# Optimization experiments

Measured on AMD Instinct MI355X. Metric: run time of the kernel, lower is better.

Reference implementation:

```python
import jax, jax.numpy as jnp
import numpy as np

B, T, C = 4, 2048, 2048
H = 16
D = C // H  # 128


def setup_inputs() -> dict:
    key = jax.random.key(0)
    ks = jax.random.split(key, 9)
    s = 0.02
    return {
        "x": jax.random.normal(ks[0], (B, T, C), dtype=jnp.float32),
        "wq": jax.random.normal(ks[1], (C, C), dtype=jnp.float32) * s,
        "bq": jax.random.normal(ks[2], (C,), dtype=jnp.float32) * s,
        "wk": jax.random.normal(ks[3], (C, C), dtype=jnp.float32) * s,
        "bk": jax.random.normal(ks[4], (C,), dtype=jnp.float32) * s,
        "wv": jax.random.normal(ks[5], (C, C), dtype=jnp.float32) * s,
        "bv": jax.random.normal(ks[6], (C,), dtype=jnp.float32) * s,
        "wo": jax.random.normal(ks[7], (C, C), dtype=jnp.float32) * s,
        "bo": jax.random.normal(ks[8], (C,), dtype=jnp.float32) * s,
    }


def reference(x, wq, bq, wk, bk, wv, bv, wo, bo):
    Bz, Tz, Cz = x.shape
    # projections (torch Linear: x @ W^T + b)
    q = (x @ wq.T + bq).reshape(Bz, Tz, H, D).transpose(0, 2, 1, 3)  # [B,H,T,D]
    k = (x @ wk.T + bk).reshape(Bz, Tz, H, D).transpose(0, 2, 1, 3)
    v = (x @ wv.T + bv).reshape(Bz, Tz, H, D).transpose(0, 2, 1, 3)
    scale = 1.0 / jnp.sqrt(jnp.float32(D))
    scores = jnp.einsum("bhqd,bhkd->bhqk", q, k) * scale  # [B,H,T,T]
    causal = jnp.tril(jnp.ones((Tz, Tz), dtype=bool))
    scores = jnp.where(causal, scores, jnp.float32(-jnp.inf))
    att = jax.nn.softmax(scores, axis=-1)
    out = jnp.einsum("bhqk,bhkd->bhqd", att, v)  # [B,H,T,D]
    out = out.transpose(0, 2, 1, 3).reshape(Bz, Tz, Cz)
    out = out @ wo.T + bo
    return out
```

## Files before the change

### kernel.cpp

```cpp
#include <hip/hip_runtime.h>
#include <hip/hip_bf16.h>

typedef float  f32x4  __attribute__((ext_vector_type(4)));
typedef __bf16 bf16x8 __attribute__((ext_vector_type(8)));
typedef __bf16 bf16x4 __attribute__((ext_vector_type(4)));

#define Bz 4
#define Tz 2048
#define Cz 2048
#define Hh 16
#define Dd 128
#define Mm 8192

__device__ __forceinline__ void gload_lds16(const __bf16* g, __bf16* l) {
  __builtin_amdgcn_global_load_lds(
      (const __attribute__((address_space(1))) void*)g,
      (__attribute__((address_space(3))) void*)l, 16, 0, 0);
}

__global__ __launch_bounds__(256)
void cvt_bf16(const float* __restrict__ in, __bf16* __restrict__ out, int n8) {
  int i = blockIdx.x * 256 + threadIdx.x;
  if (i >= n8) return;
  size_t base = (size_t)i * 8;
  f32x4 a = *(const f32x4*)(in + base);
  f32x4 b = *(const f32x4*)(in + base + 4);
  bf16x8 o;
  o[0]=(__bf16)a[0]; o[1]=(__bf16)a[1]; o[2]=(__bf16)a[2]; o[3]=(__bf16)a[3];
  o[4]=(__bf16)b[0]; o[5]=(__bf16)b[1]; o[6]=(__bf16)b[2]; o[7]=(__bf16)b[3];
  *(bf16x8*)(out + base) = o;
}

template<int MODE>
__global__ __launch_bounds__(512, 2)
void gemm_bt(const __bf16* __restrict__ A, const __bf16* __restrict__ W,
             const float* __restrict__ bias, void* __restrict__ Out,
             int K, float scale)
{
  __shared__ __bf16 As[2][256 * 64];
  __shared__ __bf16 Bs[2][256 * 64];

  const int tid  = threadIdx.x;
  const int lane = tid & 63;
  const int wave = tid >> 6;
  const int wm = wave >> 2, wn = wave & 3;
  const int g  = lane >> 4;
  const int lr = lane & 15;
  const int row0 = blockIdx.x * 256;
  const int col0 = blockIdx.y * 256;

  #define STG(MAT, PTR, base0, kofs, buf)                                \
    _Pragma("unroll")                                                    \
    for (int q = 0; q < 4; ++q) {                                        \
      const int r  = q * 64 + (tid >> 3);                                \
      const int cb = (tid & 7) ^ (r & 7);                                \
      gload_lds16(PTR + (size_t)(base0 + r) * K + (kofs) + cb * 8,       \
                  &MAT[buf][(q * 64 + wave * 8) * 64]);                  \
    }

  f32x4 acc[8][4] = {};

  STG(As, A, row0, 0, 0);
  STG(Bs, W, col0, 0, 0);
  asm volatile("s_waitcnt vmcnt(0)" ::: "memory");
  asm volatile("s_barrier" ::: "memory");

  const int NT = K >> 6;
  bf16x8 bfr[4][2];
  for (int kt = 0; kt < NT; ++kt) {
    const int d  = kt & 1;
    const bool pf = (kt + 1 < NT);
    const int kn = (kt + 1) << 6;

    #pragma unroll
    for (int p = 0; p < 4; ++p) {
      if (p == 0) {
        #pragma unroll
        for (int n = 0; n < 4; ++n)
          #pragma unroll
          for (int kk = 0; kk < 2; ++kk) {
            const int br = wn * 64 + n * 16 + lr;
            bfr[n][kk] = *(const bf16x8*)(&Bs[d][br * 64 + ((((kk << 2) | g) ^ (br & 7)) << 3)]);
          }
      }
      bf16x8 af[2][2];
      #pragma unroll
      for (int mf = 0; mf < 2; ++mf)
        #pragma unroll
        for (int kk = 0; kk < 2; ++kk) {
          const int ar = wm * 128 + (p * 2 + mf) * 16 + lr;
          af[mf][kk] = *(const bf16x8*)(&As[d][ar * 64 + ((((kk << 2) | g) ^ (ar & 7)) << 3)]);
        }
      if (pf && p == 0) STG(As, A, row0, kn, d ^ 1);
      if (pf && p == 1) STG(Bs, W, col0, kn, d ^ 1);

      asm volatile("s_barrier" ::: "memory");
      __builtin_amdgcn_s_setprio(1);
      #pragma unroll
      for (int kk = 0; kk < 2; ++kk)
        #pragma unroll
        for (int mf = 0; mf < 2; ++mf)
          #pragma unroll
          for (int n = 0; n < 4; ++n)
            acc[p * 2 + mf][n] = __builtin_amdgcn_mfma_f32_16x16x32_bf16(
                af[mf][kk], bfr[n][kk], acc[p * 2 + mf][n], 0, 0, 0);
      __builtin_amdgcn_s_setprio(0);
      if (p == 3) asm volatile("s_waitcnt vmcnt(0)" ::: "memory");
      asm volatile("s_barrier" ::: "memory");
    }
  }
  #undef STG

  #pragma unroll
  for (int j = 0; j < 4; ++j) {
    const int col = col0 + wn * 64 + j * 16 + lr;
    const float bv = bias[col];
    #pragma unroll
    for (int i = 0; i < 8; ++i) {
      if (MODE == 2) {
        const int row = row0 + wm * 128 + i * 16 + g * 4;
        const int b = row >> 11, t = row & (Tz - 1);
        const int h = col >> 7,  d = col & (Dd - 1);
        bf16x4 v4;
        #pragma unroll
        for (int r = 0; r < 4; ++r) v4[r] = (__bf16)(acc[i][j][r] + bv);
        *(bf16x4*)((__bf16*)Out + ((size_t)(b * Hh + h) * Dd + d) * Tz + t) = v4;
      } else {
        #pragma unroll
        for (int r = 0; r < 4; ++r) {
          const int row = row0 + wm * 128 + i * 16 + g * 4 + r;
          const float v = acc[i][j][r] + bv;
          if (MODE == 0) {
            const int b = row >> 11, t = row & (Tz - 1);
            const int h = col >> 7,  d = col & (Dd - 1);
            ((__bf16*)Out)[((size_t)(b * Hh + h) * Tz + t) * Dd + d] = (__bf16)(v * scale);
          } else {
            ((float*)Out)[(size_t)row * Cz + col] = v;
          }
        }
      }
    }
  }
}

__global__ __launch_bounds__(256, 2)
void attn_fwd(const __bf16* __restrict__ Q, const __bf16* __restrict__ Kg,
              const __bf16* __restrict__ Vt, __bf16* __restrict__ O)
{
  __shared__ __bf16 Ks[2][64 * 128];
  __shared__ __bf16 Vs[2][128 * 64];
  __shared__ __bf16 Ps[4][32 * 64];

  const int tid  = threadIdx.x;
  const int lane = tid & 63;
  const int wave = tid >> 6;
  const int g  = lane >> 4;
  const int lr = lane & 15;
  const int pair = blockIdx.y;
  const int b = pair >> 4, h = pair & 15;

  const __bf16* Qp = Q  + (size_t)pair * Tz * Dd;
  const __bf16* Kp = Kg + (size_t)pair * Tz * Dd;
  const __bf16* Vp = Vt + (size_t)pair * Dd * Tz;

  #define STAGE_KV(kv0_, buf_)                                                  \
    {                                                                           \
      const int kv0s = (kv0_);                                                  \
      _Pragma("unroll")                                                         \
      for (int p = 0; p < 4; ++p) {                                             \
        const int r  = p * 16 + wave * 4 + (lane >> 4);                         \
        const int cb = (lane & 15) ^ (r & 7);                                   \
        gload_lds16(Kp + (size_t)(kv0s + r) * Dd + cb * 8,                      \
                    &Ks[buf_][p * 2048 + wave * 512]);                          \
        const int d  = p * 32 + wave * 8 + (lane >> 3);                         \
        const int cv = (lane & 7) ^ (d & 7);                                    \
        gload_lds16(Vp + (size_t)d * Tz + kv0s + cv * 8,                        \
                    &Vs[buf_][p * 2048 + wave * 512]);                          \
      }                                                                         \
    }

  for (int pass = 0; pass < 2; ++pass) {
    const int qt  = pass == 0 ? (15 - (int)blockIdx.x) : (int)blockIdx.x;
    const int qw0 = qt * 128 + wave * 32;

    bf16x8 qf[2][4];
    #pragma unroll
    for (int im = 0; im < 2; ++im)
      #pragma unroll
      for (int ks = 0; ks < 4; ++ks)
        qf[im][ks] = *(const bf16x8*)(Qp + (size_t)(qw0 + im*16 + lr) * Dd + ks*32 + g*8);

    f32x4 oacc[2][8] = {};
    float mrow[2], lsum[2];
    mrow[0] = mrow[1] = -1e30f;
    lsum[0] = lsum[1] = 0.f;

    const int ntiles = 2 * qt + 2;

    STAGE_KV(0, 0);
    __syncthreads();

    for (int kt = 0; kt < ntiles; ++kt) {
      const int cur = kt & 1;
      const int kv0 = kt * 64;
      if (kt + 1 < ntiles) STAGE_KV((kt + 1) * 64, cur ^ 1);

      if (kv0 <= qw0 + 31) {
        f32x4 sacc[2][4] = {};
        __builtin_amdgcn_s_setprio(1);
        #pragma unroll
        for (int ks = 0; ks < 4; ++ks) {
          bf16x8 kf[4];
          #pragma unroll
          for (int in = 0; in < 4; ++in) {
            const int r = in*16 + lr;
            kf[in] = *(const bf16x8*)(&Ks[cur][r * 128 + ((((ks<<2)|g) ^ (r & 7)) << 3)]);
          }
          #pragma unroll
          for (int im = 0; im < 2; ++im)
            #pragma unroll
            for (int in = 0; in < 4; ++in)
              sacc[im][in] = __builtin_amdgcn_mfma_f32_16x16x32_bf16(kf[in], qf[im][ks], sacc[im][in], 0, 0, 0);
        }
        __builtin_amdgcn_s_setprio(0);

        if (kv0 + 63 > qw0) {
          #pragma unroll
          for (int im = 0; im < 2; ++im) {
            const int q = qw0 + im*16 + lr;
            #pragma unroll
            for (int in = 0; in < 4; ++in)
              #pragma unroll
              for (int r = 0; r < 4; ++r) {
                const int kv = kv0 + in*16 + g*4 + r;
                if (kv > q) sacc[im][in][r] = -3e38f;
              }
          }
        }

        #pragma unroll
        for (int im = 0; im < 2; ++im) {
          float m = fmaxf(fmaxf(sacc[im][0][0], sacc[im][0][1]),
                          fmaxf(sacc[im][0][2], sacc[im][0][3]));
          #pragma unroll
          for (int in = 1; in < 4; ++in)
            m = fmaxf(m, fmaxf(fmaxf(sacc[im][in][0], sacc[im][in][1]),
                               fmaxf(sacc[im][in][2], sacc[im][in][3])));
          m = fmaxf(m, __shfl_xor(m, 16));
          m = fmaxf(m, __shfl_xor(m, 32));

          const bool need = m > mrow[im] + 11.54f;
          if (__any(need)) {
            const float mn   = need ? m : mrow[im];
            const float corr = __builtin_amdgcn_exp2f(mrow[im] - mn);
            mrow[im] = mn;
            lsum[im] *= corr;
            const int sb = 20 * g;
            const float c0 = __shfl(corr, sb + 0);
            const float c1 = __shfl(corr, sb + 1);
            const float c2 = __shfl(corr, sb + 2);
            const float c3 = __shfl(corr, sb + 3);
            #pragma unroll
            for (int dn = 0; dn < 8; ++dn) {
              oacc[im][dn][0] *= c0; oacc[im][dn][1] *= c1;
              oacc[im][dn][2] *= c2; oacc[im][dn][3] *= c3;
            }
          }

          float rs = 0.f;
          const int prow = im*16 + lr;
          #pragma unroll
          for (int in = 0; in < 4; ++in) {
            const float p0 = __builtin_amdgcn_exp2f(sacc[im][in][0] - mrow[im]);
            const float p1 = __builtin_amdgcn_exp2f(sacc[im][in][1] - mrow[im]);
            const float p2 = __builtin_amdgcn_exp2f(sacc[im][in][2] - mrow[im]);
            const float p3 = __builtin_amdgcn_exp2f(sacc[im][in][3] - mrow[im]);
            rs += (p0 + p1) + (p2 + p3);
            bf16x4 q4;
            q4[0] = (__bf16)p0; q4[1] = (__bf16)p1;
            q4[2] = (__bf16)p2; q4[3] = (__bf16)p3;
            const int bs = (in*4 + g) ^ ((prow & 3) << 2);
            *(bf16x4*)(&Ps[wave][prow * 64 + bs * 4]) = q4;
          }
          rs += __shfl_xor(rs, 16);
          rs += __shfl_xor(rs, 32);
          lsum[im] += rs;
        }

        __builtin_amdgcn_s_setprio(1);
        #pragma unroll
        for (int kk = 0; kk < 2; ++kk) {
          bf16x8 pa[2];
          #pragma unroll
          for (int im = 0; im < 2; ++im) {
            const int prow = im*16 + lr;
            const int bs = (kk*8 + 2*g) ^ ((prow & 3) << 2);
            pa[im] = *(const bf16x8*)(&Ps[wave][prow * 64 + bs * 4]);
          }
          #pragma unroll
          for (int dn = 0; dn < 8; ++dn) {
            const int d = dn*16 + lr;
            bf16x8 vb = *(const bf16x8*)(&Vs[cur][d * 64 + ((((kk<<2)|g) ^ (d & 7)) << 3)]);
            #pragma unroll
            for (int im = 0; im < 2; ++im)
              oacc[im][dn] = __builtin_amdgcn_mfma_f32_16x16x32_bf16(pa[im], vb, oacc[im][dn], 0, 0, 0);
          }
        }
        __builtin_amdgcn_s_setprio(0);
      }
      __syncthreads();
    }

    #pragma unroll
    for (int im = 0; im < 2; ++im) {
      const float inv = 1.0f / lsum[im];
      const int sb = 20 * g;
      const float i0 = __shfl(inv, sb + 0);
      const float i1 = __shfl(inv, sb + 1);
      const float i2 = __shfl(inv, sb + 2);
      const float i3 = __shfl(inv, sb + 3);
      #pragma unroll
      for (int dn = 0; dn < 8; ++dn) {
        const int qrow = qw0 + im*16 + g*4;
        const int d    = h * Dd + dn*16 + lr;
        O[((size_t)(b * Tz + qrow + 0)) * Cz + d] = (__bf16)(oacc[im][dn][0] * i0);
        O[((size_t)(b * Tz + qrow + 1)) * Cz + d] = (__bf16)(oacc[im][dn][1] * i1);
        O[((size_t)(b * Tz + qrow + 2)) * Cz + d] = (__bf16)(oacc[im][dn][2] * i2);
        O[((size_t)(b * Tz + qrow + 3)) * Cz + d] = (__bf16)(oacc[im][dn][3] * i3);
      }
    }
  }
  #undef STAGE_KV
}

extern "C" void kernel_launch(void* const* d_in, const int* in_sizes, int n_in,
                              void* d_out, int out_size, void* d_ws, size_t ws_size,
                              hipStream_t stream) {
  const float* x  = (const float*)d_in[0];
  const float* wq = (const float*)d_in[1];
  const float* bq = (const float*)d_in[2];
  const float* wk = (const float*)d_in[3];
  const float* bk = (const float*)d_in[4];
  const float* wv = (const float*)d_in[5];
  const float* bv = (const float*)d_in[6];
  const float* wo = (const float*)d_in[7];
  const float* bo = (const float*)d_in[8];
  float* out = (float*)d_out;

  char* w = (char*)d_ws;
  __bf16* xb   = (__bf16*)w; w += (size_t)Mm * Cz * 2;
  __bf16* wbuf = (__bf16*)w; w += (size_t)Cz * Cz * 2;
  __bf16* qb   = (__bf16*)w; w += (size_t)Mm * Cz * 2;
  __bf16* kb   = (__bf16*)w; w += (size_t)Mm * Cz * 2;
  __bf16* vbuf = (__bf16*)w; w += (size_t)Mm * Cz * 2;
  if (ws_size < (size_t)(w - (char*)d_ws)) return;

  const int nx8 = Mm * Cz / 8;
  const int nw8 = Cz * Cz / 8;
  dim3 ggrid(Mm / 256, Cz / 256);
  const float qscale = 0.12752551286084110f;

  cvt_bf16<<<nx8 / 256, 256, 0, stream>>>(x, xb, nx8);

  cvt_bf16<<<nw8 / 256, 256, 0, stream>>>(wq, wbuf, nw8);
  gemm_bt<0><<<ggrid, 512, 0, stream>>>(xb, wbuf, bq, qb, Cz, qscale);

  cvt_bf16<<<nw8 / 256, 256, 0, stream>>>(wk, wbuf, nw8);
  gemm_bt<0><<<ggrid, 512, 0, stream>>>(xb, wbuf, bk, kb, Cz, 1.0f);

  cvt_bf16<<<nw8 / 256, 256, 0, stream>>>(wv, wbuf, nw8);
  gemm_bt<2><<<ggrid, 512, 0, stream>>>(xb, wbuf, bv, vbuf, Cz, 1.0f);

  __bf16* ob = xb;
  attn_fwd<<<dim3(8, Bz * Hh), 256, 0, stream>>>(qb, kb, vbuf, ob);

  cvt_bf16<<<nw8 / 256, 256, 0, stream>>>(wo, wbuf, nw8);
  gemm_bt<1><<<ggrid, 512, 0, stream>>>(ob, wbuf, bo, out, Cz, 1.0f);
}
```

Before: 423.0 us.

## Restructure GEMM LDS staging into per-half buffers with two-stage-ahead prefetch

The GEMM's LDS tiles are split into 128-row halves, so each wave group loads only the half it consumes. Global-to-LDS loads are now issued two k-tiles ahead, with a partial vmcnt wait, instead of one tile ahead inside the compute phases. The goal is to hide more global memory latency and keep loads off the MFMA phases. The cost is an extra barrier and vmcnt wait after each k-tile, plus more loads in flight.

```diff
diff --git a/kernel.cpp b/kernel.cpp
--- a/kernel.cpp
+++ b/kernel.cpp
@@ -37,8 +37,8 @@
              const float* __restrict__ bias, void* __restrict__ Out,
              int K, float scale)
 {
-  __shared__ __bf16 As[2][256 * 64];
-  __shared__ __bf16 Bs[2][256 * 64];
+  __shared__ __bf16 Ah[4][128 * 64];
+  __shared__ __bf16 Bh[4][128 * 64];
 
   const int tid  = threadIdx.x;
   const int lane = tid & 63;
@@ -49,29 +49,37 @@
   const int row0 = blockIdx.x * 256;
   const int col0 = blockIdx.y * 256;
 
-  #define STG(MAT, PTR, base0, kofs, buf)                                \
-    _Pragma("unroll")                                                    \
-    for (int q = 0; q < 4; ++q) {                                        \
-      const int r  = q * 64 + (tid >> 3);                                \
-      const int cb = (tid & 7) ^ (r & 7);                                \
-      gload_lds16(PTR + (size_t)(base0 + r) * K + (kofs) + cb * 8,       \
-                  &MAT[buf][(q * 64 + wave * 8) * 64]);                  \
+  const int hb  = wn >> 1;
+  const int sbB = wm * 2 + (wn & 1);
+  const int cbl = ((lane & 7) ^ (lane >> 3)) << 3;
+  const int rlA = lane >> 3;
+
+  #define STAGE(s_)                                                          \
+    {                                                                        \
+      const int buf_ = (((s_) & 1) << 1);                                    \
+      const int ko_  = (s_) << 6;                                            \
+      _Pragma("unroll")                                                      \
+      for (int j = 0; j < 4; ++j) {                                          \
+        const int rA_ = wn * 32 + j * 8;                                     \
+        gload_lds16(A + (size_t)(row0 + wm * 128 + rA_ + rlA) * K + ko_ + cbl,\
+                    &Ah[buf_ + wm][rA_ * 64]);                               \
+        const int rB_ = sbB * 32 + j * 8;                                    \
+        gload_lds16(W + (size_t)(col0 + hb * 128 + rB_ + rlA) * K + ko_ + cbl,\
+                    &Bh[buf_ + hb][rB_ * 64]);                               \
+      }                                                                      \
     }
 
   f32x4 acc[8][4] = {};
-
-  STG(As, A, row0, 0, 0);
-  STG(Bs, W, col0, 0, 0);
-  asm volatile("s_waitcnt vmcnt(0)" ::: "memory");
+  const int NT = K >> 6;
+
+  STAGE(0);
+  STAGE(1);
+  asm volatile("s_waitcnt vmcnt(8)" ::: "memory");
   asm volatile("s_barrier" ::: "memory");
 
-  const int NT = K >> 6;
   bf16x8 bfr[4][2];
-  for (int kt = 0; kt < NT; ++kt) {
-    const int d  = kt & 1;
-    const bool pf = (kt + 1 < NT);
-    const int kn = (kt + 1) << 6;
-
+  for (int s = 0; s < NT; ++s) {
+    const int pa = (s & 1) << 1;
     #pragma unroll
     for (int p = 0; p < 4; ++p) {
       if (p == 0) {
@@ -79,8 +87,8 @@
         for (int n = 0; n < 4; ++n)
           #pragma unroll
           for (int kk = 0; kk < 2; ++kk) {
-            const int br = wn * 64 + n * 16 + lr;
-            bfr[n][kk] = *(const bf16x8*)(&Bs[d][br * 64 + ((((kk << 2) | g) ^ (br & 7)) << 3)]);
+            const int br = (wn & 1) * 64 + n * 16 + lr;
+            bfr[n][kk] = *(const bf16x8*)(&Bh[pa + hb][br * 64 + ((((kk << 2) | g) ^ (br & 7)) << 3)]);
           }
       }
       bf16x8 af[2][2];
@@ -88,12 +96,9 @@
       for (int mf = 0; mf < 2; ++mf)
         #pragma unroll
         for (int kk = 0; kk < 2; ++kk) {
-          const int ar = wm * 128 + (p * 2 + mf) * 16 + lr;
-          af[mf][kk] = *(const bf16x8*)(&As[d][ar * 64 + ((((kk << 2) | g) ^ (ar & 7)) << 3)]);
-        }
-      if (pf && p == 0) STG(As, A, row0, kn, d ^ 1);
-      if (pf && p == 1) STG(Bs, W, col0, kn, d ^ 1);
-
+          const int ar = (p * 2 + mf) * 16 + lr;
+          af[mf][kk] = *(const bf16x8*)(&Ah[pa + wm][ar * 64 + ((((kk << 2) | g) ^ (ar & 7)) << 3)]);
+        }
       asm volatile("s_barrier" ::: "memory");
       __builtin_amdgcn_s_setprio(1);
       #pragma unroll
@@ -105,11 +110,17 @@
             acc[p * 2 + mf][n] = __builtin_amdgcn_mfma_f32_16x16x32_bf16(
                 af[mf][kk], bfr[n][kk], acc[p * 2 + mf][n], 0, 0, 0);
       __builtin_amdgcn_s_setprio(0);
-      if (p == 3) asm volatile("s_waitcnt vmcnt(0)" ::: "memory");
       asm volatile("s_barrier" ::: "memory");
     }
+    if (s + 2 < NT) {
+      STAGE(s + 2);
+      asm volatile("s_waitcnt vmcnt(8)" ::: "memory");
+    } else {
+      asm volatile("s_waitcnt vmcnt(0)" ::: "memory");
+    }
+    asm volatile("s_barrier" ::: "memory");
   }
-  #undef STG
+  #undef STAGE
 
   #pragma unroll
   for (int j = 0; j < 4; ++j) {
```

New measurement: 466.1 us. 1.1x slower.
